# Performance work log

Measured on AMD Instinct MI355X. Metric: run time of the kernel, lower is better.

Reference implementation:

```python
import jax, jax.numpy as jnp
import numpy as np

B, I, O, ORDER = 16384, 256, 256, 8
LO, HI = -1.0, 1.0


def setup_inputs() -> dict:
    key = jax.random.key(0)
    k1, k2, k3 = jax.random.split(key, 3)
    x = jax.random.normal(k1, (B, I), dtype=jnp.float32)
    weights = jax.random.normal(k2, (O, I), dtype=jnp.float32)
    # BernsteinBasisFunction init: randn(order+1) * 0.1, one per (o, i) pair
    coeffs = jax.random.normal(k3, (O, I, ORDER + 1), dtype=jnp.float32) * 0.1
    return {"x": x, "weights": weights, "coeffs": coeffs}


def reference(x, weights, coeffs):
    # x: [B, I]; weights: [O, I]; coeffs: [O, I, K+1]
    K = coeffs.shape[-1] - 1
    zoom = (HI - LO) / 2.0
    pan = (HI + LO) / 2.0
    xt = jnp.tanh(x) * zoom + pan          # squash into [LO, HI]
    x_a = xt - LO                          # [B, I]
    x_b = HI - xt                          # [B, I]
    e = jnp.arange(K + 1)
    # ber[b, i, k] = x_a^k * x_b^(K-k)  (unnormalized Bernstein basis)
    ber = (x_a[..., None] ** e) * (x_b[..., None] ** (K - e))  # [B, I, K+1]
    # transformed[b, o, i] = sum_k coeffs[o,i,k] * ber[b,i,k]; out = einsum('boi,oi->bo')
    # Fused: fold weights into coeffs to avoid the [B, O, I] intermediate.
    wc = coeffs * weights[..., None]       # [O, I, K+1]
    return jnp.einsum('bik,oik->bo', ber, wc)
```

## Files before the change

kernel.cpp:

```cpp
#include <hip/hip_runtime.h>
#include <hip/hip_bf16.h>


#define BDIM 16384
#define IDIM 256
#define ODIM 256
#define NK 9
#define NCHUNK 4
#define NSTEP 36
#define STEP_ELEMS (ODIM * 64)

typedef short short8 __attribute__((ext_vector_type(8)));
typedef float floatx4 __attribute__((ext_vector_type(4)));

__global__ __launch_bounds__(256) void prep_wc2(const float* __restrict__ weights,
                                                const float* __restrict__ coeffs,
                                                ushort* __restrict__ wc) {
    int idx  = blockIdx.x * 256 + threadIdx.x;
    int step = idx >> 11;
    int c    = idx & 2047;
    int big    = c >> 6;
    int lane_w = c & 63;
    int o    = (big >> 1) * 16 + (lane_w & 15);
    int s    = big & 1;
    int quad = lane_w >> 4;
    int ic = step / 9;
    int k  = step - ic * 9;
    int i0 = ic * 64 + s * 32 + quad * 8;

    const float* cp = coeffs + (size_t)(o * IDIM + i0) * NK + k;
    float4 w0 = *(const float4*)(weights + o * IDIM + i0);
    float4 w1 = *(const float4*)(weights + o * IDIM + i0 + 4);
    float wv[8] = {w0.x, w0.y, w0.z, w0.w, w1.x, w1.y, w1.z, w1.w};

    union { ushort us[8]; int4 v; __hip_bfloat162 h2[4]; } pk;
#pragma unroll
    for (int j = 0; j < 8; j += 2) {
        float a = cp[(size_t)j * NK] * wv[j];
        float b = cp[(size_t)(j + 1) * NK] * wv[j + 1];
        pk.h2[j >> 1] = __float22bfloat162_rn(make_float2(a, b));
    }
    *(int4*)(wc + (size_t)step * STEP_ELEMS + (size_t)c * 8) = pk.v;
}

__global__ __launch_bounds__(512, 2) void bern_gemm(const float* __restrict__ x,
                                                    const ushort* __restrict__ wc,
                                                    float* __restrict__ out) {
    const int tid  = threadIdx.x;
    const int wave = tid >> 6;
    const int lane = tid & 63;
    const int cg   = blockIdx.x & 3;
    const int rb   = (blockIdx.x >> 2) * 256 + wave * 32;
    const int lrow = lane & 15;
    const int jseg = (lane >> 4) * 8;

    float p[2][2][8];
    float r[2][2][8];
    floatx4 acc[2][4];
    floatx4 zero = {0.0f, 0.0f, 0.0f, 0.0f};
#pragma unroll
    for (int m = 0; m < 2; ++m)
#pragma unroll
        for (int n = 0; n < 4; ++n)
            acc[m][n] = zero;

#define LOAD_X(ic_)                                                             \
    {                                                                           \
        _Pragma("unroll") for (int m = 0; m < 2; ++m)                           \
        _Pragma("unroll") for (int s = 0; s < 2; ++s) {                         \
            const float* xp = x + (size_t)(rb + m * 16 + lrow) * IDIM           \
                              + (ic_) * 64 + s * 32 + jseg;                     \
            float4 v0 = *(const float4*)(xp);                                   \
            float4 v1 = *(const float4*)(xp + 4);                               \
            p[m][s][0] = v0.x; p[m][s][1] = v0.y;                               \
            p[m][s][2] = v0.z; p[m][s][3] = v0.w;                               \
            p[m][s][4] = v1.x; p[m][s][5] = v1.y;                               \
            p[m][s][6] = v1.z; p[m][s][7] = v1.w;                               \
        }                                                                       \
    }

#define SETUP_BASIS()                                                           \
    {                                                                           \
        _Pragma("unroll") for (int m = 0; m < 2; ++m)                           \
        _Pragma("unroll") for (int s = 0; s < 2; ++s)                           \
        _Pragma("unroll") for (int e = 0; e < 8; ++e) {                         \
            float t  = __builtin_amdgcn_exp2f(p[m][s][e] * 2.8853900817779268f);\
            float q  = 2.0f * __builtin_amdgcn_rcpf(t + 1.0f);                  \
            float q2 = q * q;                                                   \
            float q4 = q2 * q2;                                                 \
            p[m][s][e] = q4 * q4;                                               \
            r[m][s][e] = t;                                                     \
        }                                                                       \
    }

    LOAD_X(0);
    SETUP_BASIS();

    short8 bfr[2][2][4];
#pragma unroll
    for (int s = 0; s < 2; ++s)
#pragma unroll
        for (int n = 0; n < 4; ++n)
            bfr[0][s][n] = *(const short8*)(wc + (((cg * 4 + n) * 2 + s) * 64 + lane) * 8);

#pragma unroll
    for (int ic = 0; ic < NCHUNK; ++ic) {
#pragma unroll
        for (int k = 0; k < NK; ++k) {
            const int step = ic * NK + k;
            const int cur  = step & 1;
            const int nxt  = cur ^ 1;

            if (step + 1 < NSTEP) {
                const ushort* wnp = wc + (size_t)(step + 1) * STEP_ELEMS;
#pragma unroll
                for (int s = 0; s < 2; ++s)
#pragma unroll
                    for (int n = 0; n < 4; ++n)
                        bfr[nxt][s][n] = *(const short8*)(wnp + (((cg * 4 + n) * 2 + s) * 64 + lane) * 8);
            }

#pragma unroll
            for (int s = 0; s < 2; ++s)
#pragma unroll
                for (int m = 0; m < 2; ++m) {
                    union { ushort us[8]; short8 v; __hip_bfloat162 h2[4]; } pk;
#pragma unroll
                    for (int e = 0; e < 8; e += 2) {
                        pk.h2[e >> 1] = __float22bfloat162_rn(
                            make_float2(p[m][s][e], p[m][s][e + 1]));
                    }
#pragma unroll
                    for (int n = 0; n < 4; ++n)
                        acc[m][n] = __builtin_amdgcn_mfma_f32_16x16x32_bf16(
                            pk.v, bfr[cur][s][n], acc[m][n], 0, 0, 0);
                    if (k < NK - 1)
#pragma unroll
                        for (int e = 0; e < 8; ++e) p[m][s][e] *= r[m][s][e];
                }
        }

        if (ic < NCHUNK - 1) {
            LOAD_X(ic + 1);
            SETUP_BASIS();
        }
    }

#pragma unroll
    for (int m = 0; m < 2; ++m) {
#pragma unroll
        for (int n = 0; n < 4; ++n) {
            int col   = cg * 64 + n * 16 + (lane & 15);
            int rbase = rb + m * 16 + (lane >> 4) * 4;
#pragma unroll
            for (int reg = 0; reg < 4; ++reg) {
                out[(size_t)(rbase + reg) * ODIM + col] = acc[m][n][reg];
            }
        }
    }
#undef LOAD_X
#undef SETUP_BASIS
}

extern "C" void kernel_launch(void* const* d_in, const int* in_sizes, int n_in,
                              void* d_out, int out_size, void* d_ws, size_t ws_size,
                              hipStream_t stream) {
    const float* x       = (const float*)d_in[0];
    const float* weights = (const float*)d_in[1];
    const float* coeffs  = (const float*)d_in[2];
    float* out = (float*)d_out;
    ushort* wc = (ushort*)d_ws;

    prep_wc2<<<288, 256, 0, stream>>>(weights, coeffs, wc);
    bern_gemm<<<256, 512, 0, stream>>>(x, wc, out);
}
```

Baseline: 106.8 us.

## Shrink per-wave tile to 16 rows and launch more smaller blocks

Each wave now computes a 16x64 output tile instead of 32x64, with 256-thread blocks and 1024 blocks in place of 512-thread blocks and 256 blocks. Block index decoding is reordered so consecutive blocks share a column group. Halving the accumulators and basis registers should allow more waves per CU to hide latency. In exchange, every B-fragment load from the wc buffer now feeds half as many MFMAs, and the outer chunk loop is no longer unrolled.

New measurement: 366.0 us. 3.43x slower.

```diff
diff --git a/kernel.cpp b/kernel.cpp
--- a/kernel.cpp
+++ b/kernel.cpp
@@ -43,68 +43,63 @@
     *(int4*)(wc + (size_t)step * STEP_ELEMS + (size_t)c * 8) = pk.v;
 }
 
-__global__ __launch_bounds__(512, 2) void bern_gemm(const float* __restrict__ x,
+__global__ __launch_bounds__(256, 4) void bern_gemm(const float* __restrict__ x,
                                                     const ushort* __restrict__ wc,
                                                     float* __restrict__ out) {
     const int tid  = threadIdx.x;
     const int wave = tid >> 6;
     const int lane = tid & 63;
-    const int cg   = blockIdx.x & 3;
-    const int rb   = (blockIdx.x >> 2) * 256 + wave * 32;
+    const int cg   = blockIdx.x >> 8;
+    const int rb   = (blockIdx.x & 255) * 64 + wave * 16;
     const int lrow = lane & 15;
     const int jseg = (lane >> 4) * 8;
 
-    float p[2][2][8];
-    float r[2][2][8];
-    floatx4 acc[2][4];
+    float p[2][8];
+    float r[2][8];
+    floatx4 acc[4];
     floatx4 zero = {0.0f, 0.0f, 0.0f, 0.0f};
 #pragma unroll
-    for (int m = 0; m < 2; ++m)
-#pragma unroll
-        for (int n = 0; n < 4; ++n)
-            acc[m][n] = zero;
+    for (int n = 0; n < 4; ++n) acc[n] = zero;
 
 #define LOAD_X(ic_)                                                             \
     {                                                                           \
-        _Pragma("unroll") for (int m = 0; m < 2; ++m)                           \
         _Pragma("unroll") for (int s = 0; s < 2; ++s) {                         \
-            const float* xp = x + (size_t)(rb + m * 16 + lrow) * IDIM           \
+            const float* xp = x + (size_t)(rb + lrow) * IDIM                    \
                               + (ic_) * 64 + s * 32 + jseg;                     \
             float4 v0 = *(const float4*)(xp);                                   \
             float4 v1 = *(const float4*)(xp + 4);                               \
-            p[m][s][0] = v0.x; p[m][s][1] = v0.y;                               \
-            p[m][s][2] = v0.z; p[m][s][3] = v0.w;                               \
-            p[m][s][4] = v1.x; p[m][s][5] = v1.y;                               \
-            p[m][s][6] = v1.z; p[m][s][7] = v1.w;                               \
+            p[s][0] = v0.x; p[s][1] = v0.y; p[s][2] = v0.z; p[s][3] = v0.w;     \
+            p[s][4] = v1.x; p[s][5] = v1.y; p[s][6] = v1.z; p[s][7] = v1.w;     \
         }                                                                       \
     }
 
 #define SETUP_BASIS()                                                           \
     {                                                                           \
-        _Pragma("unroll") for (int m = 0; m < 2; ++m)                           \
         _Pragma("unroll") for (int s = 0; s < 2; ++s)                           \
         _Pragma("unroll") for (int e = 0; e < 8; ++e) {                         \
-            float t  = __builtin_amdgcn_exp2f(p[m][s][e] * 2.8853900817779268f);\
+            float t  = __builtin_amdgcn_exp2f(p[s][e] * 2.8853900817779268f);   \
             float q  = 2.0f * __builtin_amdgcn_rcpf(t + 1.0f);                  \
             float q2 = q * q;                                                   \
             float q4 = q2 * q2;                                                 \
-            p[m][s][e] = q4 * q4;                                               \
-            r[m][s][e] = t;                                                     \
+            p[s][e] = q4 * q4;                                                  \
+            r[s][e] = t;                                                        \
         }                                                                       \
     }
 
     LOAD_X(0);
     SETUP_BASIS();
 
+    const ushort* wbase = wc + ((size_t)(cg * 8) * 64 + lane) * 8;
+
     short8 bfr[2][2][4];
 #pragma unroll
     for (int s = 0; s < 2; ++s)
 #pragma unroll
         for (int n = 0; n < 4; ++n)
-            bfr[0][s][n] = *(const short8*)(wc + (((cg * 4 + n) * 2 + s) * 64 + lane) * 8);
+            bfr[0][s][n] = *(const short8*)(wbase + (n * 2 + s) * 512);
 
-#pragma unroll
     for (int ic = 0; ic < NCHUNK; ++ic) {
+        const ushort* wchunk = wbase + (size_t)ic * NK * STEP_ELEMS;
 #pragma unroll
         for (int k = 0; k < NK; ++k) {
             const int step = ic * NK + k;
@@ -112,32 +107,30 @@
             const int nxt  = cur ^ 1;
 
             if (step + 1 < NSTEP) {
-                const ushort* wnp = wc + (size_t)(step + 1) * STEP_ELEMS;
+                const ushort* wnp = wchunk + (size_t)(k + 1) * STEP_ELEMS;
 #pragma unroll
                 for (int s = 0; s < 2; ++s)
 #pragma unroll
                     for (int n = 0; n < 4; ++n)
-                        bfr[nxt][s][n] = *(const short8*)(wnp + (((cg * 4 + n) * 2 + s) * 64 + lane) * 8);
+                        bfr[nxt][s][n] = *(const short8*)(wnp + (n * 2 + s) * 512);
             }
 
 #pragma unroll
-            for (int s = 0; s < 2; ++s)
+            for (int s = 0; s < 2; ++s) {
+                union { ushort us[8]; short8 v; __hip_bfloat162 h2[4]; } pk;
 #pragma unroll
-                for (int m = 0; m < 2; ++m) {
-                    union { ushort us[8]; short8 v; __hip_bfloat162 h2[4]; } pk;
+                for (int e = 0; e < 8; e += 2) {
+                    pk.h2[e >> 1] = __float22bfloat162_rn(
+                        make_float2(p[s][e], p[s][e + 1]));
+                }
 #pragma unroll
-                    for (int e = 0; e < 8; e += 2) {
-                        pk.h2[e >> 1] = __float22bfloat162_rn(
-                            make_float2(p[m][s][e], p[m][s][e + 1]));
-                    }
+                for (int n = 0; n < 4; ++n)
+                    acc[n] = __builtin_amdgcn_mfma_f32_16x16x32_bf16(
+                        pk.v, bfr[cur][s][n], acc[n], 0, 0, 0);
+                if (k < NK - 1)
 #pragma unroll
-                    for (int n = 0; n < 4; ++n)
-                        acc[m][n] = __builtin_amdgcn_mfma_f32_16x16x32_bf16(
-                            pk.v, bfr[cur][s][n], acc[m][n], 0, 0, 0);
-                    if (k < NK - 1)
-#pragma unroll
-                        for (int e = 0; e < 8; ++e) p[m][s][e] *= r[m][s][e];
-                }
+                    for (int e = 0; e < 8; ++e) p[s][e] *= r[s][e];
+            }
         }
 
         if (ic < NCHUNK - 1) {
@@ -147,15 +140,12 @@
     }
 
 #pragma unroll
-    for (int m = 0; m < 2; ++m) {
+    for (int n = 0; n < 4; ++n) {
+        int col   = cg * 64 + n * 16 + (lane & 15);
+        int rbase = rb + (lane >> 4) * 4;
 #pragma unroll
-        for (int n = 0; n < 4; ++n) {
-            int col   = cg * 64 + n * 16 + (lane & 15);
-            int rbase = rb + m * 16 + (lane >> 4) * 4;
-#pragma unroll
-            for (int reg = 0; reg < 4; ++reg) {
-                out[(size_t)(rbase + reg) * ODIM + col] = acc[m][n][reg];
-            }
+        for (int reg = 0; reg < 4; ++reg) {
+            out[(size_t)(rbase + reg) * ODIM + col] = acc[n][reg];
         }
     }
 #undef LOAD_X
@@ -172,5 +162,5 @@
     ushort* wc = (ushort*)d_ws;
 
     prep_wc2<<<288, 256, 0, stream>>>(weights, coeffs, wc);
-    bern_gemm<<<256, 512, 0, stream>>>(x, wc, out);
+    bern_gemm<<<1024, 256, 0, stream>>>(x, wc, out);
 }
```

## Stage B-operand weights into LDS via async global_load_lds double buffering

Applied to the files above, without the earlier changes.

Each block now copies the bf16 weight-coefficient tiles into a double-buffered 64KB shared-memory area, four K-steps at a time, using direct global-to-LDS loads. Waves then read their MFMA B fragments from LDS instead of each wave fetching them from global memory into registers. The loop is restructured into 9 groups of 4 steps with a __syncthreads per group. This shares B loads across the 8 waves and frees register double-buffers, at the cost of added barriers, LDS traffic and a possible occupancy limit from the 64KB LDS per block.

New measurement: 97.80 us. 8.4% less time.

```diff
diff --git a/kernel.cpp b/kernel.cpp
--- a/kernel.cpp
+++ b/kernel.cpp
@@ -9,6 +9,7 @@
 #define NCHUNK 4
 #define NSTEP 36
 #define STEP_ELEMS (ODIM * 64)
+#define CGW 4
 
 typedef short short8 __attribute__((ext_vector_type(8)));
 typedef float floatx4 __attribute__((ext_vector_type(4)));
@@ -46,6 +47,8 @@
 __global__ __launch_bounds__(512, 2) void bern_gemm(const float* __restrict__ x,
                                                     const ushort* __restrict__ wc,
                                                     float* __restrict__ out) {
+    __shared__ ushort Blds[2][16384];
+
     const int tid  = threadIdx.x;
     const int wave = tid >> 6;
     const int lane = tid & 63;
@@ -93,35 +96,45 @@
         }                                                                       \
     }
 
+#define STAGE(g_, b_)                                                           \
+    {                                                                           \
+        _Pragma("unroll") for (int q = 0; q < 4; ++q) {                         \
+            int st  = (g_) * 4 + q;                                             \
+            const ushort* sp = wc + (size_t)st * STEP_ELEMS + cg * 4096         \
+                               + wave * 512 + lane * 8;                         \
+            ushort* dp = &Blds[b_][(q * 8 + wave) * 512 + lane * 8];            \
+            __builtin_amdgcn_global_load_lds(                                   \
+                (const __attribute__((address_space(1))) void*)sp,              \
+                (__attribute__((address_space(3))) void*)dp, 16, 0, 0);         \
+        }                                                                       \
+    }
+
     LOAD_X(0);
     SETUP_BASIS();
-
-    short8 bfr[2][2][4];
-#pragma unroll
-    for (int s = 0; s < 2; ++s)
-#pragma unroll
-        for (int n = 0; n < 4; ++n)
-            bfr[0][s][n] = *(const short8*)(wc + (((cg * 4 + n) * 2 + s) * 64 + lane) * 8);
+    STAGE(0, 0);
 
 #pragma unroll
-    for (int ic = 0; ic < NCHUNK; ++ic) {
-#pragma unroll
-        for (int k = 0; k < NK; ++k) {
-            const int step = ic * NK + k;
-            const int cur  = step & 1;
-            const int nxt  = cur ^ 1;
-
-            if (step + 1 < NSTEP) {
-                const ushort* wnp = wc + (size_t)(step + 1) * STEP_ELEMS;
-#pragma unroll
-                for (int s = 0; s < 2; ++s)
-#pragma unroll
-                    for (int n = 0; n < 4; ++n)
-                        bfr[nxt][s][n] = *(const short8*)(wnp + (((cg * 4 + n) * 2 + s) * 64 + lane) * 8);
-            }
+    for (int g = 0; g < 9; ++g) {
+        __syncthreads();
+        if (g < 8) STAGE(g + 1, (g + 1) & 1);
 
 #pragma unroll
-            for (int s = 0; s < 2; ++s)
+        for (int k4 = 0; k4 < 4; ++k4) {
+            const int step = g * 4 + k4;
+            if (step == 9 || step == 18 || step == 27) {
+                LOAD_X(step / 9);
+                SETUP_BASIS();
+            }
+            const int kin = step % 9;
+
+#pragma unroll
+            for (int s = 0; s < 2; ++s) {
+                short8 bfr[4];
+#pragma unroll
+                for (int n = 0; n < 4; ++n)
+                    bfr[n] = *(const short8*)&Blds[g & 1]
+                        [k4 * 4096 + (n * 2 + s) * 512 + lane * 8];
+
 #pragma unroll
                 for (int m = 0; m < 2; ++m) {
                     union { ushort us[8]; short8 v; __hip_bfloat162 h2[4]; } pk;
@@ -133,16 +146,12 @@
 #pragma unroll
                     for (int n = 0; n < 4; ++n)
                         acc[m][n] = __builtin_amdgcn_mfma_f32_16x16x32_bf16(
-                            pk.v, bfr[cur][s][n], acc[m][n], 0, 0, 0);
-                    if (k < NK - 1)
+                            pk.v, bfr[n], acc[m][n], 0, 0, 0);
+                    if (kin < NK - 1)
 #pragma unroll
                         for (int e = 0; e < 8; ++e) p[m][s][e] *= r[m][s][e];
                 }
-        }
-
-        if (ic < NCHUNK - 1) {
-            LOAD_X(ic + 1);
-            SETUP_BASIS();
+            }
         }
     }
 
@@ -160,6 +169,7 @@
     }
 #undef LOAD_X
 #undef SETUP_BASIS
+#undef STAGE
 }
 
 extern "C" void kernel_launch(void* const* d_in, const int* in_sizes, int n_in,
```
